# Optimization experiments

Hardware: AMD Instinct MI355X
Metric: run time of the kernel (lower is better)

The kernel has to match this reference:

```python
import jax, jax.numpy as jnp
import numpy as np

N_NODES = 50000
N_EDGES = 1600000
IN_NF, IN_EF, H1, H2, OUT_NF = 64, 16, 32, 32, 64
MH1, MH2, MH3 = 64, 128, 64


def _linear_params(key, fan_in, fan_out):
    kw, kb = jax.random.split(key)
    s = 1.0 / np.sqrt(fan_in)
    W = jax.random.uniform(kw, (fan_in, fan_out), minval=-s, maxval=s, dtype=jnp.float32)
    b = jax.random.uniform(kb, (fan_out,), minval=-s, maxval=s, dtype=jnp.float32)
    return W, b


def setup_inputs() -> dict:
    key = jax.random.key(0)
    ks = jax.random.split(key, 12)
    nf = jax.random.normal(ks[0], (N_NODES, IN_NF), dtype=jnp.float32)
    ef = jax.random.normal(ks[1], (N_EDGES, IN_EF), dtype=jnp.float32)
    src = jax.random.randint(ks[2], (N_EDGES,), 0, N_NODES)
    dst = jax.random.randint(ks[3], (N_EDGES,), 0, N_NODES)
    # MLP_msg: (2*in_nf+in_ef) -> 64 -> 128 -> 64 -> (1+h1+h2)
    Wm1, bm1 = _linear_params(ks[4], 2 * IN_NF + IN_EF, MH1)
    Wm2, bm2 = _linear_params(ks[5], MH1, MH2)
    Wm3, bm3 = _linear_params(ks[6], MH2, MH3)
    Wm4, bm4 = _linear_params(ks[7], MH3, 1 + H1 + H2)
    # MLP_reduce: (in_nf+h1+h2) -> 64 -> 128 -> 64 -> out_nf
    Wr1, br1 = _linear_params(ks[8], IN_NF + H1 + H2, MH1)
    Wr2, br2 = _linear_params(ks[9], MH1, MH2)
    Wr3, br3 = _linear_params(ks[10], MH2, MH3)
    Wr4, br4 = _linear_params(ks[11], MH3, OUT_NF)
    return {"nf": nf, "ef": ef, "src": src, "dst": dst,
            "Wm1": Wm1, "bm1": bm1, "Wm2": Wm2, "bm2": bm2,
            "Wm3": Wm3, "bm3": bm3, "Wm4": Wm4, "bm4": bm4,
            "Wr1": Wr1, "br1": br1, "Wr2": Wr2, "br2": br2,
            "Wr3": Wr3, "br3": br3, "Wr4": Wr4, "br4": br4}


def _mlp(x, Ws, bs):
    n = len(Ws)
    for i, (W, b) in enumerate(zip(Ws, bs)):
        x = x @ W + b
        if i < n - 1:
            x = jax.nn.leaky_relu(x, negative_slope=0.2)
    return x


def reference(nf, ef, src, dst,
              Wm1, bm1, Wm2, bm2, Wm3, bm3, Wm4, bm4,
              Wr1, br1, Wr2, br2, Wr3, br3, Wr4, br4):
    # edge_udf: gather src/dst node feats + edge feats, per-edge MLP, sigmoid gate
    x = jnp.concatenate([nf[src], nf[dst], ef], axis=1)  # [E, 2*in_nf+in_ef]
    x = _mlp(x, [Wm1, Wm2, Wm3, Wm4], [bm1, bm2, bm3, bm4])  # [E, 1+h1+h2]
    k = jax.nn.sigmoid(x[:, :1])
    ef1 = x[:, 1:1 + H1] * k
    ef2 = x[:, 1 + H1:] * k
    # update_all: scatter-sum of ef1, scatter-max of ef2 onto destination nodes
    nf1 = jax.ops.segment_sum(ef1, dst, num_segments=N_NODES)
    nf2 = jax.ops.segment_max(ef2, dst, num_segments=N_NODES)
    nf2 = jnp.where(jnp.isfinite(nf2), nf2, 0.0)  # DGL fills 0 for nodes with no in-edges
    y = jnp.concatenate([nf, nf1, nf2], axis=1)  # [N, in_nf+h1+h2]
    return _mlp(y, [Wr1, Wr2, Wr3, Wr4], [br1, br2, br3, br4])
```

## Files before the change

### kernel.cpp

```cpp
#include <hip/hip_runtime.h>

typedef unsigned int u32;
typedef __attribute__((ext_vector_type(8))) short short8;
typedef __attribute__((ext_vector_type(4))) short short4v;
typedef __attribute__((ext_vector_type(4))) float f32x4;

__device__ __forceinline__ float lrelu(float x){ return x > 0.f ? x : 0.2f*x; }

__device__ __forceinline__ void atomicMaxF(float* a, float v){
  if (__float_as_int(v) >= 0) atomicMax((int*)a, __float_as_int(v));
  else                        atomicMin((u32*)a, __float_as_uint(v));
}

__global__ void init_ws(float* __restrict__ nf1, float* __restrict__ nf2, int n32){
  int i = blockIdx.x*blockDim.x + threadIdx.x;
  int st = gridDim.x*blockDim.x;
  for (; i < n32; i += st){ nf1[i] = 0.f; nf2[i] = -__builtin_inff(); }
}

struct HL { short hi, lo; };
__device__ __forceinline__ HL split1(float x){
  u32 u = __float_as_uint(x);
  u32 r = u + 0x7FFFu + ((u >> 16) & 1u);
  float l = x - __uint_as_float(r & 0xFFFF0000u);
  HL o; o.hi = (short)(r >> 16); o.lo = (short)(__float_as_uint(l) >> 16);
  return o;
}

__device__ __forceinline__ void gatherB(const float* __restrict__ W, int K, int Nout,
                                        int kbase, int n, short8& hi, short8& lo){
  #pragma unroll
  for (int j = 0; j < 8; ++j){
    int k = kbase + j;
    float w = (k < K && n < Nout) ? W[(size_t)k * Nout + n] : 0.f;
    HL s = split1(w); hi[j] = s.hi; lo[j] = s.lo;
  }
}

__device__ __forceinline__ f32x4 mfma3(short8 ah, short8 al, short8 bh, short8 bl, f32x4 c){
  c = __builtin_amdgcn_mfma_f32_16x16x32_bf16(ah, bh, c, 0, 0, 0);
  c = __builtin_amdgcn_mfma_f32_16x16x32_bf16(al, bh, c, 0, 0, 0);
  c = __builtin_amdgcn_mfma_f32_16x16x32_bf16(ah, bl, c, 0, 0, 0);
  return c;
}

__device__ __forceinline__ void sstore1(short* hp, short* lp, int idx, float x){
  HL s = split1(x); hp[idx] = s.hi; lp[idx] = s.lo;
}
__device__ __forceinline__ void sstore4(short* hp, short* lp, int idx, f32x4 v){
  short4v h, l;
  #pragma unroll
  for (int j = 0; j < 4; ++j){ HL s = split1(v[j]); h[j] = s.hi; l[j] = s.lo; }
  *(short4v*)(hp + idx) = h;
  *(short4v*)(lp + idx) = l;
}

#define XS   168
#define H1S  72
#define H2S  136
#define OFF_XL   5376
#define OFF_H2H  0
#define OFF_H2L  4352
#define OFF_H1H  10752
#define OFF_H1L  13056
#define OFF_DST  15360
#define LDS_SHORTS 15488
#define LDS_BYTES  (LDS_SHORTS*2)

__global__ __launch_bounds__(256, 2) void edge_mfma(
    const float* __restrict__ nf, const float* __restrict__ ef,
    const int* __restrict__ src, const int* __restrict__ dst,
    const float* __restrict__ Wm1, const float* __restrict__ bm1,
    const float* __restrict__ Wm2, const float* __restrict__ bm2,
    const float* __restrict__ Wm3, const float* __restrict__ bm3,
    const float* __restrict__ Wm4, const float* __restrict__ bm4,
    float* __restrict__ nf1, float* __restrict__ nf2, int E)
{
  extern __shared__ short smem[];
  short* Xh  = smem;
  short* Xl  = smem + OFF_XL;
  short* H2h = smem + OFF_H2H;
  short* H2l = smem + OFF_H2L;
  short* H1h = smem + OFF_H1H;
  short* H1l = smem + OFF_H1L;
  int*  dstI = (int*)(smem + OFF_DST);

  const int lane = threadIdx.x & 63, wv = threadIdx.x >> 6;
  const int nl = lane & 15, quad = lane >> 4;
  const int nb1 = wv;
  const int slot = wv*4 + quad;

  short8 B1h[5], B1l[5];
  #pragma unroll
  for (int kc = 0; kc < 5; ++kc) gatherB(Wm1, 144, 64,  kc*32 + quad*8, nb1*16 + nl, B1h[kc], B1l[kc]);
  short8 B2h[2][2], B2l[2][2];
  #pragma unroll
  for (int i = 0; i < 2; ++i)
    #pragma unroll
    for (int kc = 0; kc < 2; ++kc) gatherB(Wm2, 64, 128, kc*32 + quad*8, (nb1 + i*4)*16 + nl, B2h[i][kc], B2l[i][kc]);
  short8 B3h[4], B3l[4];
  #pragma unroll
  for (int kc = 0; kc < 4; ++kc) gatherB(Wm3, 128, 64,  kc*32 + quad*8, nb1*16 + nl, B3h[kc], B3l[kc]);
  short8 B4h[2], B4l[2];
  #pragma unroll
  for (int kc = 0; kc < 2; ++kc) gatherB(Wm4, 64, 65, kc*32 + quad*8, nb1*16 + nl, B4h[kc], B4l[kc]);
  const int gcol = (nl < 8) ? 0 : 64;
  short8 Bgh[2], Bgl[2];
  #pragma unroll
  for (int kc = 0; kc < 2; ++kc) gatherB(Wm4, 64, 65, kc*32 + quad*8, gcol, Bgh[kc], Bgl[kc]);

  const float bi1  = bm1[nb1*16 + nl];
  const float bi2a = bm2[nb1*16 + nl], bi2b = bm2[(nb1+4)*16 + nl];
  const float bi3  = bm3[nb1*16 + nl];
  const float bi4a = bm4[nb1*16 + nl];
  const float big  = bm4[gcol];

  const int ntiles = (E + 31) >> 5;
  int pp = 0;
  for (int t = blockIdx.x; t < ntiles; t += gridDim.x, pp ^= 1){
    #pragma unroll
    for (int r2 = 0; r2 < 2; ++r2){
      int row = slot*2 + r2;
      int e = (t << 5) + row;
      int ec = e < E ? e : 0;
      int s = src[ec], d = dst[ec];
      f32x4 v0 = *(const f32x4*)(nf + (size_t)s*64 + nl*4);
      f32x4 v1 = *(const f32x4*)(nf + (size_t)d*64 + nl*4);
      sstore4(Xh, Xl, row*XS + nl*4,      v0);
      sstore4(Xh, Xl, row*XS + 64 + nl*4, v1);
      if (nl < 4){
        f32x4 v2 = *(const f32x4*)(ef + (size_t)ec*16 + nl*4);
        sstore4(Xh, Xl, row*XS + 128 + nl*4, v2);
      } else if (nl < 8){
        short4v z = {0,0,0,0};
        *(short4v*)(Xh + row*XS + 144 + (nl-4)*4) = z;
        *(short4v*)(Xl + row*XS + 144 + (nl-4)*4) = z;
      }
      if (nl == 5) dstI[pp*32 + row] = (e < E) ? d : -1;
    }
    __syncthreads();

    {
      f32x4 a1[2] = {{bi1,bi1,bi1,bi1},{bi1,bi1,bi1,bi1}};
      #pragma unroll
      for (int kc = 0; kc < 5; ++kc)
        #pragma unroll
        for (int mb = 0; mb < 2; ++mb){
          int ro = (mb*16 + nl)*XS + kc*32 + quad*8;
          short8 ah = *(const short8*)(Xh + ro);
          short8 al = *(const short8*)(Xl + ro);
          a1[mb] = mfma3(ah, al, B1h[kc], B1l[kc], a1[mb]);
        }
      #pragma unroll
      for (int mb = 0; mb < 2; ++mb)
        #pragma unroll
        for (int r = 0; r < 4; ++r)
          sstore1(H1h, H1l, (mb*16 + quad*4 + r)*H1S + nb1*16 + nl, lrelu(a1[mb][r]));
    }
    __syncthreads();

    {
      f32x4 a2a[2] = {{bi2a,bi2a,bi2a,bi2a},{bi2a,bi2a,bi2a,bi2a}};
      f32x4 a2b[2] = {{bi2b,bi2b,bi2b,bi2b},{bi2b,bi2b,bi2b,bi2b}};
      #pragma unroll
      for (int kc = 0; kc < 2; ++kc)
        #pragma unroll
        for (int mb = 0; mb < 2; ++mb){
          int ro = (mb*16 + nl)*H1S + kc*32 + quad*8;
          short8 ah = *(const short8*)(H1h + ro);
          short8 al = *(const short8*)(H1l + ro);
          a2a[mb] = mfma3(ah, al, B2h[0][kc], B2l[0][kc], a2a[mb]);
          a2b[mb] = mfma3(ah, al, B2h[1][kc], B2l[1][kc], a2b[mb]);
        }
      #pragma unroll
      for (int mb = 0; mb < 2; ++mb)
        #pragma unroll
        for (int r = 0; r < 4; ++r){
          int row = mb*16 + quad*4 + r;
          sstore1(H2h, H2l, row*H2S + nb1*16 + nl,     lrelu(a2a[mb][r]));
          sstore1(H2h, H2l, row*H2S + (nb1+4)*16 + nl, lrelu(a2b[mb][r]));
        }
    }
    __syncthreads();

    {
      f32x4 a3[2] = {{bi3,bi3,bi3,bi3},{bi3,bi3,bi3,bi3}};
      #pragma unroll
      for (int kc = 0; kc < 4; ++kc)
        #pragma unroll
        for (int mb = 0; mb < 2; ++mb){
          int ro = (mb*16 + nl)*H2S + kc*32 + quad*8;
          short8 ah = *(const short8*)(H2h + ro);
          short8 al = *(const short8*)(H2l + ro);
          a3[mb] = mfma3(ah, al, B3h[kc], B3l[kc], a3[mb]);
        }
      #pragma unroll
      for (int mb = 0; mb < 2; ++mb)
        #pragma unroll
        for (int r = 0; r < 4; ++r)
          sstore1(H1h, H1l, (mb*16 + quad*4 + r)*H1S + nb1*16 + nl, lrelu(a3[mb][r]));
    }
    __syncthreads();

    {
      f32x4 a4[2] = {{bi4a,bi4a,bi4a,bi4a},{bi4a,bi4a,bi4a,bi4a}};
      f32x4 ag[2] = {{big,big,big,big},{big,big,big,big}};
      #pragma unroll
      for (int kc = 0; kc < 2; ++kc)
        #pragma unroll
        for (int mb = 0; mb < 2; ++mb){
          int ro = (mb*16 + nl)*H1S + kc*32 + quad*8;
          short8 ah = *(const short8*)(H1h + ro);
          short8 al = *(const short8*)(H1l + ro);
          a4[mb] = mfma3(ah, al, B4h[kc], B4l[kc], a4[mb]);
          ag[mb] = mfma3(ah, al, Bgh[kc], Bgl[kc], ag[mb]);
        }
      const int n = nb1*16 + nl;
      #pragma unroll
      for (int mb = 0; mb < 2; ++mb)
        #pragma unroll
        for (int r = 0; r < 4; ++r){
          int row = mb*16 + quad*4 + r;
          float glog = __shfl(ag[mb][r], lane & 0x30);
          float g = 1.f/(1.f + __expf(-glog));
          int d = dstI[pp*32 + row];
          if (d >= 0){
            float v = a4[mb][r] * g;
            if (n >= 1 && n <= 32)  atomicAdd(nf1 + (size_t)d*32 + (n-1), v);
            else if (n >= 33)       atomicMaxF(nf2 + (size_t)d*32 + (n-33), v);
            if (nb1 == 0 && nl == 8)
              atomicMaxF(nf2 + (size_t)d*32 + 31, ag[mb][r] * g);
          }
        }
    }
  }
}

__device__ void zero_f(float* p, int n){
  for (int i = threadIdx.x; i < n; i += blockDim.x) p[i] = 0.f;
}

#define B1S 68
#define C0S 132

__device__ __forceinline__ void splitA(const float* arow, int k0, short8& hi, short8& lo){
  f32x4 x0 = *(const f32x4*)(arow + k0);
  f32x4 x1 = *(const f32x4*)(arow + k0 + 4);
  #pragma unroll
  for (int j = 0; j < 4; ++j){
    HL a = split1(x0[j]); hi[j]   = a.hi; lo[j]   = a.lo;
    HL b = split1(x1[j]); hi[4+j] = b.hi; lo[4+j] = b.lo;
  }
}

__global__ __launch_bounds__(512, 2) void node_mfma(
    const float* __restrict__ nf,
    const float* __restrict__ nf1, const float* __restrict__ nf2,
    const float* __restrict__ Wr1, const float* __restrict__ br1,
    const float* __restrict__ Wr2, const float* __restrict__ br2,
    const float* __restrict__ Wr3, const float* __restrict__ br3,
    const float* __restrict__ Wr4, const float* __restrict__ br4,
    float* __restrict__ out, int N)
{
  __shared__ float buf0[32*C0S];
  __shared__ float buf1[32*B1S];

  zero_f(buf0, 32*C0S);
  zero_f(buf1, 32*B1S);

  const int lane = threadIdx.x & 63, wv = threadIdx.x >> 6;
  const int nl = lane & 15, quad = lane >> 4;
  const int m = wv >> 2, nb = wv & 3;

  short8 B1h[4], B1l[4];
  #pragma unroll
  for (int kc = 0; kc < 4; ++kc) gatherB(Wr1, 128, 64,  kc*32 + quad*8, nb*16 + nl, B1h[kc], B1l[kc]);
  short8 B2h[2][2], B2l[2][2];
  #pragma unroll
  for (int i = 0; i < 2; ++i)
    #pragma unroll
    for (int kc = 0; kc < 2; ++kc) gatherB(Wr2, 64, 128, kc*32 + quad*8, (nb + i*4)*16 + nl, B2h[i][kc], B2l[i][kc]);
  short8 B3h[4], B3l[4];
  #pragma unroll
  for (int kc = 0; kc < 4; ++kc) gatherB(Wr3, 128, 64,  kc*32 + quad*8, nb*16 + nl, B3h[kc], B3l[kc]);
  short8 B4h[2], B4l[2];
  #pragma unroll
  for (int kc = 0; kc < 2; ++kc) gatherB(Wr4, 64, 64,   kc*32 + quad*8, nb*16 + nl, B4h[kc], B4l[kc]);

  const float bi1  = br1[nb*16 + nl];
  const float bi2a = br2[nb*16 + nl], bi2b = br2[(nb+4)*16 + nl];
  const float bi3  = br3[nb*16 + nl];
  const float bi4  = br4[nb*16 + nl];
  __syncthreads();

  const int ntiles = (N + 31) >> 5;
  for (int t = blockIdx.x; t < ntiles; t += gridDim.x){
    const int base = t << 5;
    {
      int row = wv*4 + quad;
      int n = base + row;
      int nc = n < N ? n : 0;
      *(f32x4*)(buf0 + row*C0S + nl*4) = *(const f32x4*)(nf + (size_t)nc*64 + nl*4);
      if (nl < 8){
        *(f32x4*)(buf0 + row*C0S + 64 + nl*4) = *(const f32x4*)(nf1 + (size_t)nc*32 + nl*4);
      } else {
        f32x4 v = *(const f32x4*)(nf2 + (size_t)nc*32 + (nl-8)*4);
        #pragma unroll
        for (int j = 0; j < 4; ++j) if (!(v[j] >= -3.0e38f)) v[j] = 0.f;
        *(f32x4*)(buf0 + row*C0S + 96 + (nl-8)*4) = v;
      }
    }
    __syncthreads();

    f32x4 a1 = {bi1, bi1, bi1, bi1};
    {
      const float* arow = buf0 + (m*16 + nl)*C0S;
      #pragma unroll
      for (int kc = 0; kc < 4; ++kc){
        short8 ah, al; splitA(arow, kc*32 + quad*8, ah, al);
        a1 = mfma3(ah, al, B1h[kc], B1l[kc], a1);
      }
    }
    #pragma unroll
    for (int r = 0; r < 4; ++r)
      buf1[(m*16 + quad*4 + r)*B1S + nb*16 + nl] = lrelu(a1[r]);
    __syncthreads();

    f32x4 a2a = {bi2a, bi2a, bi2a, bi2a}, a2b = {bi2b, bi2b, bi2b, bi2b};
    {
      const float* arow = buf1 + (m*16 + nl)*B1S;
      #pragma unroll
      for (int kc = 0; kc < 2; ++kc){
        short8 ah, al; splitA(arow, kc*32 + quad*8, ah, al);
        a2a = mfma3(ah, al, B2h[0][kc], B2l[0][kc], a2a);
        a2b = mfma3(ah, al, B2h[1][kc], B2l[1][kc], a2b);
      }
    }
    #pragma unroll
    for (int r = 0; r < 4; ++r){
      buf0[(m*16 + quad*4 + r)*C0S + nb*16 + nl]     = lrelu(a2a[r]);
      buf0[(m*16 + quad*4 + r)*C0S + (nb+4)*16 + nl] = lrelu(a2b[r]);
    }
    __syncthreads();

    f32x4 a3 = {bi3, bi3, bi3, bi3};
    {
      const float* arow = buf0 + (m*16 + nl)*C0S;
      #pragma unroll
      for (int kc = 0; kc < 4; ++kc){
        short8 ah, al; splitA(arow, kc*32 + quad*8, ah, al);
        a3 = mfma3(ah, al, B3h[kc], B3l[kc], a3);
      }
    }
    #pragma unroll
    for (int r = 0; r < 4; ++r)
      buf1[(m*16 + quad*4 + r)*B1S + nb*16 + nl] = lrelu(a3[r]);
    __syncthreads();

    f32x4 a4 = {bi4, bi4, bi4, bi4};
    {
      const float* arow = buf1 + (m*16 + nl)*B1S;
      #pragma unroll
      for (int kc = 0; kc < 2; ++kc){
        short8 ah, al; splitA(arow, kc*32 + quad*8, ah, al);
        a4 = mfma3(ah, al, B4h[kc], B4l[kc], a4);
      }
    }
    #pragma unroll
    for (int r = 0; r < 4; ++r){
      int n = base + m*16 + quad*4 + r;
      if (n < N) out[(size_t)n*64 + nb*16 + nl] = a4[r];
    }
  }
}

extern "C" void kernel_launch(void* const* d_in, const int* in_sizes, int n_in,
                              void* d_out, int out_size, void* d_ws, size_t ws_size,
                              hipStream_t stream) {
  const float* nf  = (const float*)d_in[0];
  const float* ef  = (const float*)d_in[1];
  const int*   src = (const int*)d_in[2];
  const int*   dst = (const int*)d_in[3];

  const int N = in_sizes[0] / 64;
  const int E = in_sizes[2];

  float* nf1 = (float*)d_ws;
  float* nf2 = nf1 + (size_t)N * 32;

  static bool attr_set = false;
  if (!attr_set){
    hipFuncSetAttribute((const void*)edge_mfma,
                        hipFuncAttributeMaxDynamicSharedMemorySize, LDS_BYTES);
    attr_set = true;
  }

  init_ws<<<2048, 256, 0, stream>>>(nf1, nf2, N * 32);

  edge_mfma<<<2048, 256, LDS_BYTES, stream>>>(
      nf, ef, src, dst,
      (const float*)d_in[4],  (const float*)d_in[5],  (const float*)d_in[6],  (const float*)d_in[7],
      (const float*)d_in[8],  (const float*)d_in[9],  (const float*)d_in[10], (const float*)d_in[11],
      nf1, nf2, E);

  node_mfma<<<512, 512, 0, stream>>>(
      nf, nf1, nf2,
      (const float*)d_in[12], (const float*)d_in[13], (const float*)d_in[14], (const float*)d_in[15],
      (const float*)d_in[16], (const float*)d_in[17], (const float*)d_in[18], (const float*)d_in[19],
      (float*)d_out, N);
}
```

Before: 1.130 ms.

## Precompute per-node first-layer projections and gather them per edge

Splits the first message-MLP layer by linearity: a new node_pre kernel computes nf@Wm1[src part] and nf@Wm1[dst part] for every node into a workspace buffer P. The edge kernel then gathers and adds the two 64-wide projections and runs only the small edge-feature part of layer 1 with MFMA. This replaces the per-edge 128-wide K contraction with work per node, which is much smaller since edges outnumber nodes about 32 to 1. In exchange it needs extra workspace, has a fallback when the workspace is too small, and gathers 2x64 floats of P per edge instead of 2x64 floats of nf, so gather traffic stays about the same.

```diff
diff --git a/kernel.cpp b/kernel.cpp
--- a/kernel.cpp
+++ b/kernel.cpp
@@ -53,6 +53,250 @@
   for (int j = 0; j < 4; ++j){ HL s = split1(v[j]); h[j] = s.hi; l[j] = s.lo; }
   *(short4v*)(hp + idx) = h;
   *(short4v*)(lp + idx) = l;
+}
+
+__global__ __launch_bounds__(256, 2) void node_pre(
+    const float* __restrict__ nf, const float* __restrict__ Wm1,
+    float* __restrict__ P, int N)
+{
+  __shared__ short Xnh[32*72];
+  __shared__ short Xnl[32*72];
+
+  const int lane = threadIdx.x & 63, wv = threadIdx.x >> 6;
+  const int nl = lane & 15, quad = lane >> 4;
+  const int nb = wv;
+  const int slot = wv*4 + quad;
+
+  short8 Bah[2], Bal[2], Bbh[2], Bbl[2];
+  #pragma unroll
+  for (int kc = 0; kc < 2; ++kc){
+    gatherB(Wm1, 144, 64, kc*32 + quad*8,      nb*16 + nl, Bah[kc], Bal[kc]);
+    gatherB(Wm1, 144, 64, 64 + kc*32 + quad*8, nb*16 + nl, Bbh[kc], Bbl[kc]);
+  }
+
+  const int ntiles = (N + 31) >> 5;
+  for (int t = blockIdx.x; t < ntiles; t += gridDim.x){
+    const int base = t << 5;
+    #pragma unroll
+    for (int r2 = 0; r2 < 2; ++r2){
+      int row = slot*2 + r2;
+      int n = base + row;
+      int nc = n < N ? n : 0;
+      f32x4 v = *(const f32x4*)(nf + (size_t)nc*64 + nl*4);
+      sstore4(Xnh, Xnl, row*72 + nl*4, v);
+    }
+    __syncthreads();
+
+    f32x4 aa[2] = {{0,0,0,0},{0,0,0,0}};
+    f32x4 ab[2] = {{0,0,0,0},{0,0,0,0}};
+    #pragma unroll
+    for (int kc = 0; kc < 2; ++kc)
+      #pragma unroll
+      for (int mb = 0; mb < 2; ++mb){
+        int ro = (mb*16 + nl)*72 + kc*32 + quad*8;
+        short8 ah = *(const short8*)(Xnh + ro);
+        short8 al = *(const short8*)(Xnl + ro);
+        aa[mb] = mfma3(ah, al, Bah[kc], Bal[kc], aa[mb]);
+        ab[mb] = mfma3(ah, al, Bbh[kc], Bbl[kc], ab[mb]);
+      }
+    #pragma unroll
+    for (int mb = 0; mb < 2; ++mb)
+      #pragma unroll
+      for (int r = 0; r < 4; ++r){
+        int n = base + mb*16 + quad*4 + r;
+        if (n < N){
+          P[(size_t)n*128 +      nb*16 + nl] = aa[mb][r];
+          P[(size_t)n*128 + 64 + nb*16 + nl] = ab[mb][r];
+        }
+      }
+    __syncthreads();
+  }
+}
+
+#define PXES  40
+#define PSS   68
+#define PH1S  72
+#define PH2S  136
+#define POFF_XEL  1280
+#define POFF_S    2560
+#define POFF_H1H  6912
+#define POFF_H1L  9216
+#define POFF_H2H  11520
+#define POFF_H2L  15872
+#define POFF_DST  20224
+#define P_LDS_SHORTS 20352
+#define P_LDS_BYTES  (P_LDS_SHORTS*2)
+
+__global__ __launch_bounds__(256, 2) void edge_mfma_p(
+    const float* __restrict__ P, const float* __restrict__ ef,
+    const int* __restrict__ src, const int* __restrict__ dst,
+    const float* __restrict__ Wm1, const float* __restrict__ bm1,
+    const float* __restrict__ Wm2, const float* __restrict__ bm2,
+    const float* __restrict__ Wm3, const float* __restrict__ bm3,
+    const float* __restrict__ Wm4, const float* __restrict__ bm4,
+    float* __restrict__ nf1, float* __restrict__ nf2, int E)
+{
+  extern __shared__ short smem[];
+  short* Xeh = smem;
+  short* Xel = smem + POFF_XEL;
+  float* Sb  = (float*)(smem + POFF_S);
+  short* H1h = smem + POFF_H1H;
+  short* H1l = smem + POFF_H1L;
+  short* H2h = smem + POFF_H2H;
+  short* H2l = smem + POFF_H2L;
+  int*  dstI = (int*)(smem + POFF_DST);
+
+  {
+    float* z = (float*)smem;
+    for (int i = threadIdx.x; i < POFF_XEL; i += blockDim.x) z[i] = 0.f;
+  }
+
+  const int lane = threadIdx.x & 63, wv = threadIdx.x >> 6;
+  const int nl = lane & 15, quad = lane >> 4;
+  const int nb1 = wv;
+  const int slot = wv*4 + quad;
+
+  short8 B1ch, B1cl;
+  gatherB(Wm1, 144, 64, 128 + quad*8, nb1*16 + nl, B1ch, B1cl);
+  short8 B2h[2][2], B2l[2][2];
+  #pragma unroll
+  for (int i = 0; i < 2; ++i)
+    #pragma unroll
+    for (int kc = 0; kc < 2; ++kc) gatherB(Wm2, 64, 128, kc*32 + quad*8, (nb1 + i*4)*16 + nl, B2h[i][kc], B2l[i][kc]);
+  short8 B3h[4], B3l[4];
+  #pragma unroll
+  for (int kc = 0; kc < 4; ++kc) gatherB(Wm3, 128, 64,  kc*32 + quad*8, nb1*16 + nl, B3h[kc], B3l[kc]);
+  short8 B4h[2], B4l[2];
+  #pragma unroll
+  for (int kc = 0; kc < 2; ++kc) gatherB(Wm4, 64, 65, kc*32 + quad*8, nb1*16 + nl, B4h[kc], B4l[kc]);
+  const int gcol = (nl < 8) ? 0 : 64;
+  short8 Bgh[2], Bgl[2];
+  #pragma unroll
+  for (int kc = 0; kc < 2; ++kc) gatherB(Wm4, 64, 65, kc*32 + quad*8, gcol, Bgh[kc], Bgl[kc]);
+
+  const float bi1  = bm1[nb1*16 + nl];
+  const float bi2a = bm2[nb1*16 + nl], bi2b = bm2[(nb1+4)*16 + nl];
+  const float bi3  = bm3[nb1*16 + nl];
+  const float bi4a = bm4[nb1*16 + nl];
+  const float big  = bm4[gcol];
+  __syncthreads();
+
+  const int ntiles = (E + 31) >> 5;
+  int pp = 0;
+  for (int t = blockIdx.x; t < ntiles; t += gridDim.x, pp ^= 1){
+    #pragma unroll
+    for (int r2 = 0; r2 < 2; ++r2){
+      int row = slot*2 + r2;
+      int e = (t << 5) + row;
+      int ec = e < E ? e : 0;
+      int s = src[ec], d = dst[ec];
+      f32x4 a = *(const f32x4*)(P + (size_t)s*128 +      nl*4);
+      f32x4 b = *(const f32x4*)(P + (size_t)d*128 + 64 + nl*4);
+      f32x4 sv = a + b;
+      *(f32x4*)(Sb + row*PSS + nl*4) = sv;
+      if (nl < 4){
+        f32x4 v2 = *(const f32x4*)(ef + (size_t)ec*16 + nl*4);
+        sstore4(Xeh, Xel, row*PXES + nl*4, v2);
+      }
+      if (nl == 5) dstI[pp*32 + row] = (e < E) ? d : -1;
+    }
+    __syncthreads();
+
+    {
+      f32x4 a1[2] = {{bi1,bi1,bi1,bi1},{bi1,bi1,bi1,bi1}};
+      #pragma unroll
+      for (int mb = 0; mb < 2; ++mb){
+        int ro = (mb*16 + nl)*PXES + quad*8;
+        short8 ah = *(const short8*)(Xeh + ro);
+        short8 al = *(const short8*)(Xel + ro);
+        a1[mb] = mfma3(ah, al, B1ch, B1cl, a1[mb]);
+      }
+      #pragma unroll
+      for (int mb = 0; mb < 2; ++mb)
+        #pragma unroll
+        for (int r = 0; r < 4; ++r){
+          int row = mb*16 + quad*4 + r;
+          float sv = Sb[row*PSS + nb1*16 + nl];
+          sstore1(H1h, H1l, row*PH1S + nb1*16 + nl, lrelu(a1[mb][r] + sv));
+        }
+    }
+    __syncthreads();
+
+    {
+      f32x4 a2a[2] = {{bi2a,bi2a,bi2a,bi2a},{bi2a,bi2a,bi2a,bi2a}};
+      f32x4 a2b[2] = {{bi2b,bi2b,bi2b,bi2b},{bi2b,bi2b,bi2b,bi2b}};
+      #pragma unroll
+      for (int kc = 0; kc < 2; ++kc)
+        #pragma unroll
+        for (int mb = 0; mb < 2; ++mb){
+          int ro = (mb*16 + nl)*PH1S + kc*32 + quad*8;
+          short8 ah = *(const short8*)(H1h + ro);
+          short8 al = *(const short8*)(H1l + ro);
+          a2a[mb] = mfma3(ah, al, B2h[0][kc], B2l[0][kc], a2a[mb]);
+          a2b[mb] = mfma3(ah, al, B2h[1][kc], B2l[1][kc], a2b[mb]);
+        }
+      #pragma unroll
+      for (int mb = 0; mb < 2; ++mb)
+        #pragma unroll
+        for (int r = 0; r < 4; ++r){
+          int row = mb*16 + quad*4 + r;
+          sstore1(H2h, H2l, row*PH2S + nb1*16 + nl,     lrelu(a2a[mb][r]));
+          sstore1(H2h, H2l, row*PH2S + (nb1+4)*16 + nl, lrelu(a2b[mb][r]));
+        }
+    }
+    __syncthreads();
+
+    {
+      f32x4 a3[2] = {{bi3,bi3,bi3,bi3},{bi3,bi3,bi3,bi3}};
+      #pragma unroll
+      for (int kc = 0; kc < 4; ++kc)
+        #pragma unroll
+        for (int mb = 0; mb < 2; ++mb){
+          int ro = (mb*16 + nl)*PH2S + kc*32 + quad*8;
+          short8 ah = *(const short8*)(H2h + ro);
+          short8 al = *(const short8*)(H2l + ro);
+          a3[mb] = mfma3(ah, al, B3h[kc], B3l[kc], a3[mb]);
+        }
+      #pragma unroll
+      for (int mb = 0; mb < 2; ++mb)
+        #pragma unroll
+        for (int r = 0; r < 4; ++r)
+          sstore1(H1h, H1l, (mb*16 + quad*4 + r)*PH1S + nb1*16 + nl, lrelu(a3[mb][r]));
+    }
+    __syncthreads();
+
+    {
+      f32x4 a4[2] = {{bi4a,bi4a,bi4a,bi4a},{bi4a,bi4a,bi4a,bi4a}};
+      f32x4 ag[2] = {{big,big,big,big},{big,big,big,big}};
+      #pragma unroll
+      for (int kc = 0; kc < 2; ++kc)
+        #pragma unroll
+        for (int mb = 0; mb < 2; ++mb){
+          int ro = (mb*16 + nl)*PH1S + kc*32 + quad*8;
+          short8 ah = *(const short8*)(H1h + ro);
+          short8 al = *(const short8*)(H1l + ro);
+          a4[mb] = mfma3(ah, al, B4h[kc], B4l[kc], a4[mb]);
+          ag[mb] = mfma3(ah, al, Bgh[kc], Bgl[kc], ag[mb]);
+        }
+      const int n = nb1*16 + nl;
+      #pragma unroll
+      for (int mb = 0; mb < 2; ++mb)
+        #pragma unroll
+        for (int r = 0; r < 4; ++r){
+          int row = mb*16 + quad*4 + r;
+          float glog = __shfl(ag[mb][r], lane & 0x30);
+          float g = 1.f/(1.f + __expf(-glog));
+          int d = dstI[pp*32 + row];
+          if (d >= 0){
+            float v = a4[mb][r] * g;
+            if (n >= 1 && n <= 32)  atomicAdd(nf1 + (size_t)d*32 + (n-1), v);
+            else if (n >= 33)       atomicMaxF(nf2 + (size_t)d*32 + (n-33), v);
+            if (nb1 == 0 && nl == 8)
+              atomicMaxF(nf2 + (size_t)d*32 + 31, ag[mb][r] * g);
+          }
+        }
+    }
+  }
 }
 
 #define XS   168
@@ -387,21 +631,36 @@
 
   float* nf1 = (float*)d_ws;
   float* nf2 = nf1 + (size_t)N * 32;
+  float* P   = nf2 + (size_t)N * 32;
+
+  size_t need = (size_t)N * 64 * 4 + (size_t)N * 128 * 4;
+  bool useP = (ws_size >= need);
 
   static bool attr_set = false;
   if (!attr_set){
     hipFuncSetAttribute((const void*)edge_mfma,
                         hipFuncAttributeMaxDynamicSharedMemorySize, LDS_BYTES);
+    hipFuncSetAttribute((const void*)edge_mfma_p,
+                        hipFuncAttributeMaxDynamicSharedMemorySize, P_LDS_BYTES);
     attr_set = true;
   }
 
   init_ws<<<2048, 256, 0, stream>>>(nf1, nf2, N * 32);
 
-  edge_mfma<<<2048, 256, LDS_BYTES, stream>>>(
-      nf, ef, src, dst,
-      (const float*)d_in[4],  (const float*)d_in[5],  (const float*)d_in[6],  (const float*)d_in[7],
-      (const float*)d_in[8],  (const float*)d_in[9],  (const float*)d_in[10], (const float*)d_in[11],
-      nf1, nf2, E);
+  if (useP){
+    node_pre<<<1024, 256, 0, stream>>>(nf, (const float*)d_in[4], P, N);
+    edge_mfma_p<<<2048, 256, P_LDS_BYTES, stream>>>(
+        P, ef, src, dst,
+        (const float*)d_in[4],  (const float*)d_in[5],  (const float*)d_in[6],  (const float*)d_in[7],
+        (const float*)d_in[8],  (const float*)d_in[9],  (const float*)d_in[10], (const float*)d_in[11],
+        nf1, nf2, E);
+  } else {
+    edge_mfma<<<2048, 256, LDS_BYTES, stream>>>(
+        nf, ef, src, dst,
+        (const float*)d_in[4],  (const float*)d_in[5],  (const float*)d_in[6],  (const float*)d_in[7],
+        (const float*)d_in[8],  (const float*)d_in[9],  (const float*)d_in[10], (const float*)d_in[11],
+        nf1, nf2, E);
+  }
 
   node_mfma<<<512, 512, 0, stream>>>(
       nf, nf1, nf2,
```

New measurement: 1.126 ms. Within noise of the previous version (-0.4%).
